# Kernel optimization log

Hardware: AMD Instinct MI355X
Metric: run time of the kernel (lower is better)

## Reference

```python
import jax, jax.numpy as jnp
import numpy as np

IN_CH, IN_DIM, OUT_CH, OUT_DIM = 16, 32, 32, 32
NUM_ITERS = 3
EPS = 1e-11


def setup_inputs() -> dict:
    key = jax.random.key(0)
    kx, kw = jax.random.split(key)
    B, N = 32, 128
    x = jax.random.normal(kx, (B, N, IN_CH, IN_DIM), dtype=jnp.float32)
    # learned transform, matches torch Parameter randn(1,1,in_ch,out_ch,in_dim,out_dim)
    W = jax.random.normal(kw, (IN_CH, OUT_CH, IN_DIM, OUT_DIM), dtype=jnp.float32)
    return {"x": x, "W": W, "number_of_nodes": N}


def squash(s):
    # s: [B, 1, out_ch, out_dim]; squash along capsule dim (axis=3)
    mag_sq = jnp.sum(s * s, axis=3, keepdims=True)
    mag = jnp.sqrt(mag_sq) + EPS
    a_j = mag_sq / (1.0 + mag_sq)
    return a_j * (s / mag), a_j


def reference(x, W, number_of_nodes):
    B, N = x.shape[0], x.shape[1]
    # u_hat[b,n,c,o,j] = sum_i x[b,n,c,i] * W[c,o,i,j]
    u_hat = jnp.einsum('bnci,coij->bncoj', x, W)
    u_hat = u_hat.reshape(B, N * IN_CH, OUT_CH, OUT_DIM)

    b_ij = jnp.zeros((B, N * IN_CH, OUT_CH, 1), dtype=u_hat.dtype)
    v_j = a_j = None
    for _ in range(NUM_ITERS):
        c_ij = jax.nn.softmax(b_ij, axis=1)          # softmax over input capsules
        s_j = jnp.sum(c_ij * u_hat, axis=1, keepdims=True)  # [B,1,out_ch,out_dim]
        v_j, a_j = squash(s_j)
        # agreement: broadcast v_j over input-capsule dim (no explicit cat)
        u_vj = jnp.sum(u_hat * v_j, axis=3, keepdims=True)
        b_ij = b_ij + u_vj
    return v_j, a_j
```

## Files before the change

### kernel.cpp

```cpp
#include <hip/hip_runtime.h>
#include <math.h>

#define BB 32
#define NN 128
#define CC 16
#define OO 32
#define II 32
#define JJ 32
#define MM (NN*CC)
#define WP (JJ+1)
static constexpr float EPS_ = 1e-11f;


__global__ __launch_bounds__(1024) void k_transpose(
    const float* __restrict__ x, float* __restrict__ xT) {
  int b = blockIdx.x >> 4, c = blockIdx.x & 15;
  __shared__ __align__(16) float xsT[II][NN + 4];
  int tid = threadIdx.x;
  {
    int n = tid >> 3, i4 = (tid & 7) * 4;
    float4 v = *(const float4*)(x + (((size_t)(b * NN + n)) * CC + c) * II + i4);
    xsT[i4 + 0][n] = v.x; xsT[i4 + 1][n] = v.y;
    xsT[i4 + 2][n] = v.z; xsT[i4 + 3][n] = v.w;
  }
  __syncthreads();
  {
    int i = tid >> 5, n4 = tid & 31;
    float4 v = *(const float4*)(&xsT[i][n4 * 4]);
    ((float4*)(xT + ((size_t)(b * CC + c)) * II * NN))[tid] = v;
  }
}

__device__ __forceinline__ float rs16(float p[16], int l) {
  bool u2 = (l >> 1) & 1, u4 = (l >> 2) & 1, u8 = (l >> 3) & 1, u16 = (l >> 4) & 1;
  #pragma unroll
  for (int k = 0; k < 8; ++k) {
    float s0 = u2 ? p[k] : p[k + 8];
    float r0 = __shfl_xor(s0, 2);
    p[k] = (u2 ? p[k + 8] : p[k]) + r0;
  }
  #pragma unroll
  for (int k = 0; k < 4; ++k) {
    float s0 = u4 ? p[k] : p[k + 4];
    float r0 = __shfl_xor(s0, 4);
    p[k] = (u4 ? p[k + 4] : p[k]) + r0;
  }
  #pragma unroll
  for (int k = 0; k < 2; ++k) {
    float s0 = u8 ? p[k] : p[k + 2];
    float r0 = __shfl_xor(s0, 8);
    p[k] = (u8 ? p[k + 2] : p[k]) + r0;
  }
  {
    float s0 = u16 ? p[0] : p[1];
    float r0 = __shfl_xor(s0, 16);
    p[0] = (u16 ? p[1] : p[0]) + r0;
  }
  p[0] += __shfl_xor(p[0], 32);
  return p[0];
}

__global__ __launch_bounds__(1024, 4) void k_route(
    const float* __restrict__ xT, const float* __restrict__ W,
    float* __restrict__ out) {
  int bid = blockIdx.x;
  int b = bid & 31, o0 = (bid >> 5) * 2;
  int tid = threadIdx.x;

  __shared__ float Ws[CC * 2 * II * WP];
  __shared__ __align__(16) float bijL[2][CC][NN];
  __shared__ __align__(16) float cw[2][CC][II];
  __shared__ float partA[2][CC][JJ];
  __shared__ float vs[2][JJ];
  __shared__ float redM[CC][2], redE[CC][2];

  {
    int q = tid & 7, r0 = tid >> 3;
    #pragma unroll
    for (int k = 0; k < 8; ++k) {
      int rowid = r0 + k * 128;
      int c = rowid >> 6, o = (rowid >> 5) & 1, i = rowid & 31;
      float4 v = *(const float4*)(W + ((((size_t)c * OO + o0 + o) * II + i) * JJ) + q * 4);
      float* dst = &Ws[rowid * WP + q * 4];
      dst[0] = v.x; dst[1] = v.y; dst[2] = v.z; dst[3] = v.w;
    }
  }

  int l = tid & 63;
  int c = tid >> 6, n4 = l >> 1, s = l & 1;
  const float4* xTb = (const float4*)(xT + (size_t)b * CC * II * NN);
  const float4* xp  = xTb + c * (II * NN / 4) + (s * 16) * (NN / 4) + n4;
  float4 xv[16];
  #pragma unroll
  for (int q = 0; q < 16; ++q) xv[q] = xp[q * (NN / 4)];

  {
    int o = tid >> 9, ci = (tid >> 5) & 15, m4i = tid & 31;
    *(float4*)(&bijL[o][ci][m4i * 4]) = make_float4(0.f, 0.f, 0.f, 0.f);
  }
  float mo0 = 0.f, mo1 = 0.f;
  float rin0 = 1.0f / (float)MM, rin1 = rin0;
  __syncthreads();

  for (int it = 0; it < 3; ++it) {
    {
      int qf = ((l >> 1) & 1) * 8 + ((l >> 2) & 1) * 4
             + ((l >> 3) & 1) * 2 + ((l >> 4) & 1);
      #pragma unroll
      for (int o = 0; o < 2; ++o) {
        float4 bb = *(const float4*)(&bijL[o][c][n4 * 4]);
        float m  = (o == 0) ? mo0 : mo1;
        float ri = (o == 0) ? rin0 : rin1;
        float cfx = __expf(bb.x - m) * ri, cfy = __expf(bb.y - m) * ri;
        float cfz = __expf(bb.z - m) * ri, cfw = __expf(bb.w - m) * ri;
        float p[16];
        #pragma unroll
        for (int q = 0; q < 16; ++q)
          p[q] = xv[q].x*cfx + xv[q].y*cfy + xv[q].z*cfz + xv[q].w*cfw;
        float r = rs16(p, l);
        if ((l & 32) == 0) cw[o][c][s * 16 + qf] = r;
      }
    }

    {
      int cA = tid >> 6, o = (tid >> 5) & 1, j = tid & 31;
      const float* wsp = &Ws[((cA * 2 + o) * II) * WP + j];
      float acc = 0.f;
      #pragma unroll 8
      for (int i = 0; i < II; ++i)
        acc += cw[o][cA][i] * wsp[i * WP];
      partA[o][cA][j] = acc;
    }
    __syncthreads();

    if (tid < 64) {
      int o = tid >> 5, j = tid & 31;
      float sA = 0.f;
      #pragma unroll
      for (int cR = 0; cR < CC; ++cR) sA += partA[o][cR][j];
      float msq = sA * sA;
      #pragma unroll
      for (int off = 16; off > 0; off >>= 1) msq += __shfl_xor(msq, off);
      float mag = sqrtf(msq) + EPS_;
      float a   = msq / (1.0f + msq);
      float vvq = a * sA / mag;
      if (it == 2) {
        int row = b * OO + (o0 + o);
        out[(size_t)row * JJ + j] = vvq;
        if (j == 0) out[BB * OO * JJ + row] = a;
      } else {
        vs[o][j] = vvq;
      }
    }
    if (it == 2) break;
    __syncthreads();

    {
      int cW = tid >> 6, o = (tid >> 5) & 1, i = tid & 31;
      const float* wsr = &Ws[((cW * 2 + o) * II + i) * WP];
      float acc = 0.f;
      #pragma unroll 8
      for (int j = 0; j < JJ; ++j)
        acc += wsr[j] * vs[o][j];
      cw[o][cW][i] = acc;
    }

    {
      float4 ac0 = make_float4(0.f,0.f,0.f,0.f);
      float4 ac1 = make_float4(0.f,0.f,0.f,0.f);
      #pragma unroll
      for (int q = 0; q < 16; ++q) {
        int i = s * 16 + q;
        float w0 = cw[0][c][i], w1 = cw[1][c][i];
        ac0.x += xv[q].x * w0; ac0.y += xv[q].y * w0;
        ac0.z += xv[q].z * w0; ac0.w += xv[q].w * w0;
        ac1.x += xv[q].x * w1; ac1.y += xv[q].y * w1;
        ac1.z += xv[q].z * w1; ac1.w += xv[q].w * w1;
      }
      ac0.x += __shfl_xor(ac0.x, 1); ac0.y += __shfl_xor(ac0.y, 1);
      ac0.z += __shfl_xor(ac0.z, 1); ac0.w += __shfl_xor(ac0.w, 1);
      ac1.x += __shfl_xor(ac1.x, 1); ac1.y += __shfl_xor(ac1.y, 1);
      ac1.z += __shfl_xor(ac1.z, 1); ac1.w += __shfl_xor(ac1.w, 1);
      float4 r = (s == 0) ? ac0 : ac1;
      float4 bb = *(const float4*)(&bijL[s][c][n4 * 4]);
      r.x += bb.x; r.y += bb.y; r.z += bb.z; r.w += bb.w;
      *(float4*)(&bijL[s][c][n4 * 4]) = r;

      float m4 = fmaxf(fmaxf(r.x, r.y), fmaxf(r.z, r.w));
      #pragma unroll
      for (int off = 2; off <= 32; off <<= 1) m4 = fmaxf(m4, __shfl_xor(m4, off));
      float e = __expf(r.x - m4) + __expf(r.y - m4)
              + __expf(r.z - m4) + __expf(r.w - m4);
      #pragma unroll
      for (int off = 2; off <= 32; off <<= 1) e += __shfl_xor(e, off);
      int wave = tid >> 6;
      if ((tid & 63) <= 1) { redM[wave][s] = m4; redE[wave][s] = e; }
      __syncthreads();
      float mo = redM[0][s];
      #pragma unroll
      for (int w2 = 1; w2 < CC; ++w2) mo = fmaxf(mo, redM[w2][s]);
      float ss = 0.f;
      #pragma unroll
      for (int w2 = 0; w2 < CC; ++w2)
        ss += redE[w2][s] * __expf(redM[w2][s] - mo);
      float rin = 1.0f / ss;
      float moO = __shfl_xor(mo, 1), rinO = __shfl_xor(rin, 1);
      mo0  = (s == 0) ? mo  : moO;   mo1  = (s == 0) ? moO  : mo;
      rin0 = (s == 0) ? rin : rinO;  rin1 = (s == 0) ? rinO : rin;
    }
  }
}

extern "C" void kernel_launch(void* const* d_in, const int* in_sizes, int n_in,
                              void* d_out, int out_size, void* d_ws, size_t ws_size,
                              hipStream_t stream) {
  const float* x = (const float*)d_in[0];
  const float* W = (const float*)d_in[1];
  (void)in_sizes; (void)n_in;
  float* out = (float*)d_out; (void)out_size;

  float* xT = (float*)d_ws;
  (void)ws_size;

  k_transpose<<<BB * CC, 1024, 0, stream>>>(x, xT);
  k_route<<<BB * (OO / 2), 1024, 0, stream>>>(xT, W, out);
}
```

Measured before the change: 109.0 us.

## Route one output capsule per block instead of two, doubling grid size

Each routing block now handles a single output capsule o, so the grid doubles to 1024 blocks and each block's shared footprint roughly halves. The W tile is stored unpadded with float4 copies, and the W matvecs are split across half-waves with a shuffle or pairwise combine. A rotated j index reduces bank conflicts. Per-block x loads are now duplicated across twice as many blocks, which increases global and L2 traffic in exchange for more parallelism and occupancy.

```diff
diff --git a/kernel.cpp b/kernel.cpp
--- a/kernel.cpp
+++ b/kernel.cpp
@@ -8,7 +8,6 @@
 #define II 32
 #define JJ 32
 #define MM (NN*CC)
-#define WP (JJ+1)
 static constexpr float EPS_ = 1e-11f;
 
 
@@ -60,29 +59,27 @@
   return p[0];
 }
 
-__global__ __launch_bounds__(1024, 4) void k_route(
+__global__ __launch_bounds__(1024) void k_route(
     const float* __restrict__ xT, const float* __restrict__ W,
     float* __restrict__ out) {
   int bid = blockIdx.x;
-  int b = bid & 31, o0 = (bid >> 5) * 2;
+  int b = bid & 31, o = bid >> 5;
   int tid = threadIdx.x;
 
-  __shared__ float Ws[CC * 2 * II * WP];
-  __shared__ __align__(16) float bijL[2][CC][NN];
-  __shared__ __align__(16) float cw[2][CC][II];
-  __shared__ float partA[2][CC][JJ];
-  __shared__ float vs[2][JJ];
-  __shared__ float redM[CC][2], redE[CC][2];
-
-  {
-    int q = tid & 7, r0 = tid >> 3;
+  __shared__ float Ws[CC * II * JJ];
+  __shared__ __align__(16) float bijL[CC][NN];
+  __shared__ float cwbuf[CC * II * 2];
+  __shared__ float partA[CC][JJ];
+  __shared__ float vs[JJ];
+  __shared__ float redM[CC], redE[CC];
+
+  {
     #pragma unroll
-    for (int k = 0; k < 8; ++k) {
-      int rowid = r0 + k * 128;
-      int c = rowid >> 6, o = (rowid >> 5) & 1, i = rowid & 31;
-      float4 v = *(const float4*)(W + ((((size_t)c * OO + o0 + o) * II + i) * JJ) + q * 4);
-      float* dst = &Ws[rowid * WP + q * 4];
-      dst[0] = v.x; dst[1] = v.y; dst[2] = v.z; dst[3] = v.w;
+    for (int k = 0; k < 4; ++k) {
+      int f4i = tid + k * 1024;
+      int cc = f4i >> 8, rem = f4i & 255;
+      float4 v = *(const float4*)(W + (((size_t)(cc * OO + o)) * II) * JJ + rem * 4);
+      *(float4*)(&Ws[cc * II * JJ + rem * 4]) = v;
     }
   }
 
@@ -95,49 +92,44 @@
   for (int q = 0; q < 16; ++q) xv[q] = xp[q * (NN / 4)];
 
   {
-    int o = tid >> 9, ci = (tid >> 5) & 15, m4i = tid & 31;
-    *(float4*)(&bijL[o][ci][m4i * 4]) = make_float4(0.f, 0.f, 0.f, 0.f);
-  }
-  float mo0 = 0.f, mo1 = 0.f;
-  float rin0 = 1.0f / (float)MM, rin1 = rin0;
+    if (tid < 512) ((float4*)bijL)[tid] = make_float4(0.f, 0.f, 0.f, 0.f);
+  }
+  float mo = 0.f, rin = 1.0f / (float)MM;
   __syncthreads();
 
   for (int it = 0; it < 3; ++it) {
     {
       int qf = ((l >> 1) & 1) * 8 + ((l >> 2) & 1) * 4
              + ((l >> 3) & 1) * 2 + ((l >> 4) & 1);
-      #pragma unroll
-      for (int o = 0; o < 2; ++o) {
-        float4 bb = *(const float4*)(&bijL[o][c][n4 * 4]);
-        float m  = (o == 0) ? mo0 : mo1;
-        float ri = (o == 0) ? rin0 : rin1;
-        float cfx = __expf(bb.x - m) * ri, cfy = __expf(bb.y - m) * ri;
-        float cfz = __expf(bb.z - m) * ri, cfw = __expf(bb.w - m) * ri;
-        float p[16];
-        #pragma unroll
-        for (int q = 0; q < 16; ++q)
-          p[q] = xv[q].x*cfx + xv[q].y*cfy + xv[q].z*cfz + xv[q].w*cfw;
-        float r = rs16(p, l);
-        if ((l & 32) == 0) cw[o][c][s * 16 + qf] = r;
-      }
-    }
-
-    {
-      int cA = tid >> 6, o = (tid >> 5) & 1, j = tid & 31;
-      const float* wsp = &Ws[((cA * 2 + o) * II) * WP + j];
+      float4 bb = *(const float4*)(&bijL[c][n4 * 4]);
+      float cfx = __expf(bb.x - mo) * rin, cfy = __expf(bb.y - mo) * rin;
+      float cfz = __expf(bb.z - mo) * rin, cfw = __expf(bb.w - mo) * rin;
+      float p[16];
+      #pragma unroll
+      for (int q = 0; q < 16; ++q)
+        p[q] = xv[q].x*cfx + xv[q].y*cfy + xv[q].z*cfz + xv[q].w*cfw;
+      float r = rs16(p, l);
+      if ((l & 32) == 0) cwbuf[c * II + s * 16 + qf] = r;
+    }
+
+    {
+      int cA = tid >> 6, j = l & 31, ih = l >> 5;
+      const float* wsp = &Ws[(cA * II + ih * 16) * JJ + j];
+      const float* cxp = &cwbuf[cA * II + ih * 16];
       float acc = 0.f;
-      #pragma unroll 8
-      for (int i = 0; i < II; ++i)
-        acc += cw[o][cA][i] * wsp[i * WP];
-      partA[o][cA][j] = acc;
+      #pragma unroll
+      for (int q = 0; q < 16; ++q)
+        acc += cxp[q] * wsp[q * JJ];
+      acc += __shfl_xor(acc, 32);
+      if (ih == 0) partA[cA][j] = acc;
     }
     __syncthreads();
 
-    if (tid < 64) {
-      int o = tid >> 5, j = tid & 31;
+    if (tid < 32) {
+      int j = tid;
       float sA = 0.f;
       #pragma unroll
-      for (int cR = 0; cR < CC; ++cR) sA += partA[o][cR][j];
+      for (int cR = 0; cR < CC; ++cR) sA += partA[cR][j];
       float msq = sA * sA;
       #pragma unroll
       for (int off = 16; off > 0; off >>= 1) msq += __shfl_xor(msq, off);
@@ -145,46 +137,44 @@
       float a   = msq / (1.0f + msq);
       float vvq = a * sA / mag;
       if (it == 2) {
-        int row = b * OO + (o0 + o);
+        int row = b * OO + o;
         out[(size_t)row * JJ + j] = vvq;
         if (j == 0) out[BB * OO * JJ + row] = a;
       } else {
-        vs[o][j] = vvq;
+        vs[j] = vvq;
       }
     }
     if (it == 2) break;
     __syncthreads();
 
     {
-      int cW = tid >> 6, o = (tid >> 5) & 1, i = tid & 31;
-      const float* wsr = &Ws[((cW * 2 + o) * II + i) * WP];
+      int cW = tid >> 6, i = l & 31, jh = l >> 5;
+      const float* wsr = &Ws[(cW * II + i) * JJ];
       float acc = 0.f;
-      #pragma unroll 8
-      for (int j = 0; j < JJ; ++j)
-        acc += wsr[j] * vs[o][j];
-      cw[o][cW][i] = acc;
-    }
-
-    {
-      float4 ac0 = make_float4(0.f,0.f,0.f,0.f);
-      float4 ac1 = make_float4(0.f,0.f,0.f,0.f);
+      #pragma unroll
+      for (int jj = 0; jj < 16; ++jj) {
+        int j = jh * 16 + ((jj + i) & 15);
+        acc += wsr[j] * vs[j];
+      }
+      cwbuf[(cW * II + i) * 2 + jh] = acc;
+    }
+
+    {
+      float4 ac = make_float4(0.f, 0.f, 0.f, 0.f);
       #pragma unroll
       for (int q = 0; q < 16; ++q) {
         int i = s * 16 + q;
-        float w0 = cw[0][c][i], w1 = cw[1][c][i];
-        ac0.x += xv[q].x * w0; ac0.y += xv[q].y * w0;
-        ac0.z += xv[q].z * w0; ac0.w += xv[q].w * w0;
-        ac1.x += xv[q].x * w1; ac1.y += xv[q].y * w1;
-        ac1.z += xv[q].z * w1; ac1.w += xv[q].w * w1;
+        float w = cwbuf[(c * II + i) * 2] + cwbuf[(c * II + i) * 2 + 1];
+        ac.x += xv[q].x * w; ac.y += xv[q].y * w;
+        ac.z += xv[q].z * w; ac.w += xv[q].w * w;
       }
-      ac0.x += __shfl_xor(ac0.x, 1); ac0.y += __shfl_xor(ac0.y, 1);
-      ac0.z += __shfl_xor(ac0.z, 1); ac0.w += __shfl_xor(ac0.w, 1);
-      ac1.x += __shfl_xor(ac1.x, 1); ac1.y += __shfl_xor(ac1.y, 1);
-      ac1.z += __shfl_xor(ac1.z, 1); ac1.w += __shfl_xor(ac1.w, 1);
-      float4 r = (s == 0) ? ac0 : ac1;
-      float4 bb = *(const float4*)(&bijL[s][c][n4 * 4]);
-      r.x += bb.x; r.y += bb.y; r.z += bb.z; r.w += bb.w;
-      *(float4*)(&bijL[s][c][n4 * 4]) = r;
+      ac.x += __shfl_xor(ac.x, 1); ac.y += __shfl_xor(ac.y, 1);
+      ac.z += __shfl_xor(ac.z, 1); ac.w += __shfl_xor(ac.w, 1);
+      float4 bb = *(const float4*)(&bijL[c][n4 * 4]);
+      float4 r;
+      r.x = ac.x + bb.x; r.y = ac.y + bb.y;
+      r.z = ac.z + bb.z; r.w = ac.w + bb.w;
+      if (s == 0) *(float4*)(&bijL[c][n4 * 4]) = r;
 
       float m4 = fmaxf(fmaxf(r.x, r.y), fmaxf(r.z, r.w));
       #pragma unroll
@@ -194,19 +184,16 @@
       #pragma unroll
       for (int off = 2; off <= 32; off <<= 1) e += __shfl_xor(e, off);
       int wave = tid >> 6;
-      if ((tid & 63) <= 1) { redM[wave][s] = m4; redE[wave][s] = e; }
+      if ((tid & 63) == 0) { redM[wave] = m4; redE[wave] = e; }
       __syncthreads();
-      float mo = redM[0][s];
-      #pragma unroll
-      for (int w2 = 1; w2 < CC; ++w2) mo = fmaxf(mo, redM[w2][s]);
+      float m = redM[0];
+      #pragma unroll
+      for (int w2 = 1; w2 < CC; ++w2) m = fmaxf(m, redM[w2]);
       float ss = 0.f;
       #pragma unroll
       for (int w2 = 0; w2 < CC; ++w2)
-        ss += redE[w2][s] * __expf(redM[w2][s] - mo);
-      float rin = 1.0f / ss;
-      float moO = __shfl_xor(mo, 1), rinO = __shfl_xor(rin, 1);
-      mo0  = (s == 0) ? mo  : moO;   mo1  = (s == 0) ? moO  : mo;
-      rin0 = (s == 0) ? rin : rinO;  rin1 = (s == 0) ? rinO : rin;
+        ss += redE[w2] * __expf(redM[w2] - m);
+      mo = m; rin = 1.0f / ss;
     }
   }
 }
@@ -223,5 +210,5 @@
   (void)ws_size;
 
   k_transpose<<<BB * CC, 1024, 0, stream>>>(x, xT);
-  k_route<<<BB * (OO / 2), 1024, 0, stream>>>(xT, W, out);
-}
+  k_route<<<BB * OO, 1024, 0, stream>>>(xT, W, out);
+}
```

Result: slower. 135.0 us (+23.9%).
